# Kernel optimization log

Hardware: AMD Instinct MI355X
Metric: run time of the kernel (lower is better)

## Reference

```python
import jax, jax.numpy as jnp
import numpy as np

EPS = 1e-08  # matches torch default eps in both F.normalize and PairwiseDistance


def setup_inputs() -> dict:
    key = jax.random.key(0)
    x = jax.random.normal(key, (8192, 1024), dtype=jnp.float32)
    return {"x": x}


def reference(x) -> jnp.ndarray:
    B = x.shape[0]
    # F.normalize(x, p=2, dim=-1, eps=EPS): x / max(||x||_2, eps)
    norms = jnp.linalg.norm(x, axis=-1, keepdims=True)
    xn = x / jnp.maximum(norms, EPS)
    # cosine similarity matrix [B, B]
    cos_sim = xn @ xn.T
    # fill_diagonal_(-2): exclude self from nearest-neighbor search
    idx = jnp.arange(B)
    cos_sim = cos_sim.at[idx, idx].set(-2.0)
    nn_idx = jnp.argmax(cos_sim, axis=1)  # [B] int
    # torch PairwiseDistance(p=2, eps=EPS): ||x1 - x2 + eps||_2
    diff = xn - xn[nn_idx] + EPS
    nn_dist = jnp.sqrt(jnp.sum(diff * diff, axis=-1))  # [B]
    loss = -jnp.mean(jnp.log(nn_dist + EPS))
    return loss
```

## Files before the change

### kernel.cpp

```cpp
#include <hip/hip_runtime.h>
#include <hip/hip_bf16.h>
#include <math.h>

#define NB 8192
#define ND 1024
#define KEPS 1e-8f
#define SLOTS 128
#define NTIL 64
#define NWG 2080
#define NKT 32

typedef __attribute__((ext_vector_type(8))) __bf16 bf16x8;
typedef __attribute__((ext_vector_type(4))) float f32x4;

__device__ __forceinline__ unsigned int fmono(float f) {
    unsigned int b = __float_as_uint(f);
    return b ^ ((b & 0x80000000u) ? 0xFFFFFFFFu : 0x80000000u);
}
__device__ __forceinline__ unsigned short f2bf(float f) {
    union { float f; unsigned int u; } a;
    a.f = f;
    unsigned int lsb = (a.u >> 16) & 1u;
    a.u += 0x7fffu + lsb;
    return (unsigned short)(a.u >> 16);
}
__device__ __forceinline__ void gload_lds16(const void* g, void* l) {
    __builtin_amdgcn_global_load_lds(
        (const __attribute__((address_space(1))) unsigned int*)g,
        (__attribute__((address_space(3))) unsigned int*)l, 16, 0, 0);
}
__device__ __forceinline__ unsigned long long packmax(float mx, int mc) {
    return ((unsigned long long)fmono(mx) << 32) |
           (unsigned long long)(~(unsigned int)mc);
}

__global__ __launch_bounds__(256) void normalize_k(const float* __restrict__ x,
                                                   unsigned short* __restrict__ xnb) {
    int row = blockIdx.x * 4 + (threadIdx.x >> 6);
    int l = threadIdx.x & 63;
    const float4* xr = (const float4*)(x + (size_t)row * ND);
    float4 v[4];
    float ss = 0.f;
#pragma unroll
    for (int q = 0; q < 4; ++q) {
        v[q] = xr[q * 64 + l];
        ss += v[q].x * v[q].x + v[q].y * v[q].y + v[q].z * v[q].z + v[q].w * v[q].w;
    }
#pragma unroll
    for (int off = 1; off < 64; off <<= 1) ss += __shfl_xor(ss, off, 64);
    float scale = 1.0f / fmaxf(sqrtf(ss), KEPS);
    ushort4* o = (ushort4*)(xnb + (size_t)row * ND);
#pragma unroll
    for (int q = 0; q < 4; ++q) {
        ushort4 u;
        u.x = f2bf(v[q].x * scale);
        u.y = f2bf(v[q].y * scale);
        u.z = f2bf(v[q].z * scale);
        u.w = f2bf(v[q].w * scale);
        o[q * 64 + l] = u;
    }
}

#define FENCE_BARRIER() do { asm volatile("" ::: "memory"); \
    __builtin_amdgcn_s_barrier(); asm volatile("" ::: "memory"); } while (0)
#define WAIT_VM4() asm volatile("s_waitcnt vmcnt(4)" ::: "memory")
#define WAIT_VM0() asm volatile("s_waitcnt vmcnt(0)" ::: "memory")

#define STAGEALL(DB) do { \
    gload_lds16(spA0, ldsb + (DB) + (wv * 2 + 0) * 1024); \
    gload_lds16(spA1, ldsb + (DB) + (wv * 2 + 1) * 1024); \
    gload_lds16(spB0, ldsb + (DB) + 8192 + (wv * 2 + 0) * 1024); \
    gload_lds16(spB1, ldsb + (DB) + 8192 + (wv * 2 + 1) * 1024); \
    spA0 += 64; spA1 += 64; spB0 += 64; spB1 += 64; } while (0)

#define COMPUTE(CB) do { \
    bf16x8 af[4], bfr[4]; \
    _Pragma("unroll") for (int mi = 0; mi < 4; ++mi) \
        af[mi] = *(const bf16x8*)(ldsb + (CB) + wM * 4096 + mi * 1024 + rowks); \
    _Pragma("unroll") for (int ni = 0; ni < 4; ++ni) \
        bfr[ni] = *(const bf16x8*)(ldsb + (CB) + 8192 + wN * 4096 + ni * 1024 + rowks); \
    _Pragma("unroll") for (int mi = 0; mi < 4; ++mi) \
    _Pragma("unroll") for (int ni = 0; ni < 4; ++ni) \
        acc[mi][ni] = __builtin_amdgcn_mfma_f32_16x16x32_bf16(af[mi], bfr[ni], acc[mi][ni], 0, 0, 0); \
    } while (0)

#define KT(CB, SB) do { \
    WAIT_VM4(); FENCE_BARRIER(); STAGEALL(SB); COMPUTE(CB); } while (0)

__global__ __launch_bounds__(256, 3) void argmax_gemm(const unsigned short* __restrict__ xnb,
                                                      unsigned long long* __restrict__ partial) {
    __shared__ char ldsb[49152];

    int wg = (int)blockIdx.x;
    int tile = (wg & 7) * (NWG / 8) + (wg >> 3);
    int by = 0, tr = tile;
    while (tr >= NTIL - by) { tr -= NTIL - by; ++by; }
    const int bx = by + tr;

    const int rowBase = by * 128, colBase = bx * 128;
    const int tid = (int)threadIdx.x;
    const int wv = tid >> 6;
    const int l = tid & 63;
    const int wM = wv >> 1;
    const int wN = wv & 1;

    const int rowks = (l & 15) * 64 + (((l >> 4) * 16) ^ (((l >> 1) & 3) << 4));

    const int scol = (((l & 3) ^ ((l >> 3) & 3)) << 4);
    const char* xb = (const char*)xnb;
    const int r0 = (wv * 2 + 0) * 16 + (l >> 2);
    const int r1 = (wv * 2 + 1) * 16 + (l >> 2);
    const char* spA0 = xb + (size_t)(rowBase + r0) * 2048 + scol;
    const char* spA1 = xb + (size_t)(rowBase + r1) * 2048 + scol;
    const char* spB0 = xb + (size_t)(colBase + r0) * 2048 + scol;
    const char* spB1 = xb + (size_t)(colBase + r1) * 2048 + scol;

    f32x4 acc[4][4];
#pragma unroll
    for (int m = 0; m < 4; ++m)
#pragma unroll
        for (int n = 0; n < 4; ++n) acc[m][n] = f32x4{0.f, 0.f, 0.f, 0.f};

    STAGEALL(0);
    STAGEALL(16384);

    for (int g = 0; g < 10; ++g) {
        KT(0, 32768);
        KT(16384, 0);
        KT(32768, 16384);
    }
    WAIT_VM4(); FENCE_BARRIER(); COMPUTE(0);
    WAIT_VM0(); FENCE_BARRIER(); COMPUTE(16384);

#pragma unroll
    for (int mi = 0; mi < 4; ++mi) {
#pragma unroll
        for (int r = 0; r < 4; ++r) {
            int gi = rowBase + wM * 64 + mi * 16 + (l >> 4) * 4 + r;
            float mx = -3.0f;
            int mc = 0x7FFFFFFF;
#pragma unroll
            for (int ni = 0; ni < 4; ++ni) {
                int gj = colBase + wN * 64 + ni * 16 + (l & 15);
                float v = (gi == gj) ? -2.0f : acc[mi][ni][r];
                if (v > mx) { mx = v; mc = gj; }
            }
#pragma unroll
            for (int off = 1; off < 16; off <<= 1) {
                float omx = __shfl_xor(mx, off, 64);
                int omc = __shfl_xor(mc, off, 64);
                if (omx > mx || (omx == mx && omc < mc)) { mx = omx; mc = omc; }
            }
            if ((l & 15) == 0)
                partial[(size_t)gi * SLOTS + (bx - by) * 2 + wN] = packmax(mx, mc);
        }
    }
    if (bx > by) {
#pragma unroll
        for (int ni = 0; ni < 4; ++ni) {
            int gj = colBase + wN * 64 + ni * 16 + (l & 15);
            float mx = -3.0f;
            int mc = 0x7FFFFFFF;
#pragma unroll
            for (int mi = 0; mi < 4; ++mi) {
#pragma unroll
                for (int r = 0; r < 4; ++r) {
                    int gi = rowBase + wM * 64 + mi * 16 + (l >> 4) * 4 + r;
                    float v = (gi == gj) ? -2.0f : acc[mi][ni][r];
                    if (v > mx) { mx = v; mc = gi; }
                }
            }
#pragma unroll
            for (int off = 16; off < 64; off <<= 1) {
                float omx = __shfl_xor(mx, off, 64);
                int omc = __shfl_xor(mc, off, 64);
                if (omx > mx || (omx == mx && omc < mc)) { mx = omx; mc = omc; }
            }
            if ((l >> 4) == 0)
                partial[(size_t)gj * SLOTS + (NTIL - bx) * 2 + by * 2 + wM] = packmax(mx, mc);
        }
    }
}

__global__ __launch_bounds__(256) void dist_k(const float* __restrict__ x,
                                              const unsigned long long* __restrict__ partial,
                                              float* __restrict__ rowloss) {
    int i = blockIdx.x * 4 + (threadIdx.x >> 6);
    int l = threadIdx.x & 63;
    unsigned long long p = partial[(size_t)i * SLOTS + l];
    {
        unsigned long long o = partial[(size_t)i * SLOTS + l + 64];
        if (o > p) p = o;
    }
#pragma unroll
    for (int off = 1; off < 64; off <<= 1) {
        unsigned long long o = __shfl_xor(p, off, 64);
        if (o > p) p = o;
    }
    int j = (int)(~(unsigned int)(p & 0xFFFFFFFFull));

    const float4* xi = (const float4*)(x + (size_t)i * ND);
    const float4* xj = (const float4*)(x + (size_t)j * ND);
    float4 a[4], b[4];
    float sa = 0.f, sb = 0.f;
#pragma unroll
    for (int q = 0; q < 4; ++q) {
        a[q] = xi[q * 64 + l];
        b[q] = xj[q * 64 + l];
        sa += a[q].x * a[q].x + a[q].y * a[q].y + a[q].z * a[q].z + a[q].w * a[q].w;
        sb += b[q].x * b[q].x + b[q].y * b[q].y + b[q].z * b[q].z + b[q].w * b[q].w;
    }
#pragma unroll
    for (int off = 1; off < 64; off <<= 1) {
        sa += __shfl_xor(sa, off, 64);
        sb += __shfl_xor(sb, off, 64);
    }
    float ia = 1.0f / fmaxf(sqrtf(sa), KEPS);
    float ib = 1.0f / fmaxf(sqrtf(sb), KEPS);
    float ss = 0.f;
#pragma unroll
    for (int q = 0; q < 4; ++q) {
        float dx = a[q].x * ia - b[q].x * ib + KEPS;
        float dy = a[q].y * ia - b[q].y * ib + KEPS;
        float dz = a[q].z * ia - b[q].z * ib + KEPS;
        float dw = a[q].w * ia - b[q].w * ib + KEPS;
        ss += dx * dx + dy * dy + dz * dz + dw * dw;
    }
#pragma unroll
    for (int off = 1; off < 64; off <<= 1) ss += __shfl_xor(ss, off, 64);
    if (l == 0) rowloss[i] = -logf(sqrtf(ss) + KEPS);
}

__global__ __launch_bounds__(1024) void reduce_k(const float* __restrict__ rowloss,
                                                 float* __restrict__ out) {
    int t = threadIdx.x;
    float s = 0.0f;
#pragma unroll
    for (int k = 0; k < 8; ++k) s += rowloss[t + k * 1024];
#pragma unroll
    for (int off = 32; off > 0; off >>= 1) s += __shfl_down(s, off, 64);
    __shared__ float sred[16];
    if ((t & 63) == 0) sred[t >> 6] = s;
    __syncthreads();
    if (t == 0) {
        float tot = 0.0f;
        for (int k = 0; k < 16; ++k) tot += sred[k];
        out[0] = tot / (float)NB;
    }
}

extern "C" void kernel_launch(void* const* d_in, const int* in_sizes, int n_in,
                              void* d_out, int out_size, void* d_ws, size_t ws_size,
                              hipStream_t stream) {
    const float* x = (const float*)d_in[0];
    float* out = (float*)d_out;

    char* ws = (char*)d_ws;
    unsigned short* xnb = (unsigned short*)ws;
    unsigned long long* partial =
        (unsigned long long*)(ws + (size_t)NB * ND * 2);
    float* rowloss = (float*)(ws + (size_t)NB * ND * 2 + (size_t)NB * SLOTS * 8);

    normalize_k<<<NB / 4, 256, 0, stream>>>(x, xnb);
    argmax_gemm<<<NWG, 256, 0, stream>>>(xnb, partial);
    dist_k<<<NB / 4, 256, 0, stream>>>(x, partial, rowloss);
    reduce_k<<<1, 1024, 0, stream>>>(rowloss, out);
}
```

Measured before the change: 183.2 us.

## Compute neighbor distance algebraically from cached norms and argmax cosine value

Result: slower. 196.0 us (+7.0%).

```diff
diff --git a/kernel.cpp b/kernel.cpp
--- a/kernel.cpp
+++ b/kernel.cpp
@@ -17,6 +17,10 @@
     unsigned int b = __float_as_uint(f);
     return b ^ ((b & 0x80000000u) ? 0xFFFFFFFFu : 0x80000000u);
 }
+__device__ __forceinline__ float fmono_inv(unsigned int m) {
+    unsigned int b = (m & 0x80000000u) ? (m ^ 0x80000000u) : ~m;
+    return __uint_as_float(b);
+}
 __device__ __forceinline__ unsigned short f2bf(float f) {
     union { float f; unsigned int u; } a;
     a.f = f;
@@ -35,20 +39,28 @@
 }
 
 __global__ __launch_bounds__(256) void normalize_k(const float* __restrict__ x,
-                                                   unsigned short* __restrict__ xnb) {
+                                                   unsigned short* __restrict__ xnb,
+                                                   float2* __restrict__ sn,
+                                                   float* __restrict__ out) {
+    if (blockIdx.x == 0 && threadIdx.x == 0) out[0] = 0.0f;
     int row = blockIdx.x * 4 + (threadIdx.x >> 6);
     int l = threadIdx.x & 63;
     const float4* xr = (const float4*)(x + (size_t)row * ND);
     float4 v[4];
-    float ss = 0.f;
+    float ss = 0.f, sv = 0.f;
 #pragma unroll
     for (int q = 0; q < 4; ++q) {
         v[q] = xr[q * 64 + l];
         ss += v[q].x * v[q].x + v[q].y * v[q].y + v[q].z * v[q].z + v[q].w * v[q].w;
-    }
-#pragma unroll
-    for (int off = 1; off < 64; off <<= 1) ss += __shfl_xor(ss, off, 64);
+        sv += v[q].x + v[q].y + v[q].z + v[q].w;
+    }
+#pragma unroll
+    for (int off = 1; off < 64; off <<= 1) {
+        ss += __shfl_xor(ss, off, 64);
+        sv += __shfl_xor(sv, off, 64);
+    }
     float scale = 1.0f / fmaxf(sqrtf(ss), KEPS);
+    if (l == 0) sn[row] = make_float2(sv * scale, ss * scale * scale);
     ushort4* o = (ushort4*)(xnb + (size_t)row * ND);
 #pragma unroll
     for (int q = 0; q < 4; ++q) {
@@ -182,14 +194,14 @@
     }
 }
 
-__global__ __launch_bounds__(256) void dist_k(const float* __restrict__ x,
-                                              const unsigned long long* __restrict__ partial,
-                                              float* __restrict__ rowloss) {
+__global__ __launch_bounds__(256) void finalize_k(const unsigned long long* __restrict__ partial,
+                                                  const float2* __restrict__ sn,
+                                                  float* __restrict__ out) {
     int i = blockIdx.x * 4 + (threadIdx.x >> 6);
     int l = threadIdx.x & 63;
     unsigned long long p = partial[(size_t)i * SLOTS + l];
     {
-        unsigned long long o = partial[(size_t)i * SLOTS + l + 64];
+        unsigned long long o = partial[(size_t)i * SLOTS + 64 + l];
         if (o > p) p = o;
     }
 #pragma unroll
@@ -197,55 +209,19 @@
         unsigned long long o = __shfl_xor(p, off, 64);
         if (o > p) p = o;
     }
-    int j = (int)(~(unsigned int)(p & 0xFFFFFFFFull));
-
-    const float4* xi = (const float4*)(x + (size_t)i * ND);
-    const float4* xj = (const float4*)(x + (size_t)j * ND);
-    float4 a[4], b[4];
-    float sa = 0.f, sb = 0.f;
-#pragma unroll
-    for (int q = 0; q < 4; ++q) {
-        a[q] = xi[q * 64 + l];
-        b[q] = xj[q * 64 + l];
-        sa += a[q].x * a[q].x + a[q].y * a[q].y + a[q].z * a[q].z + a[q].w * a[q].w;
-        sb += b[q].x * b[q].x + b[q].y * b[q].y + b[q].z * b[q].z + b[q].w * b[q].w;
-    }
-#pragma unroll
-    for (int off = 1; off < 64; off <<= 1) {
-        sa += __shfl_xor(sa, off, 64);
-        sb += __shfl_xor(sb, off, 64);
-    }
-    float ia = 1.0f / fmaxf(sqrtf(sa), KEPS);
-    float ib = 1.0f / fmaxf(sqrtf(sb), KEPS);
-    float ss = 0.f;
-#pragma unroll
-    for (int q = 0; q < 4; ++q) {
-        float dx = a[q].x * ia - b[q].x * ib + KEPS;
-        float dy = a[q].y * ia - b[q].y * ib + KEPS;
-        float dz = a[q].z * ia - b[q].z * ib + KEPS;
-        float dw = a[q].w * ia - b[q].w * ib + KEPS;
-        ss += dx * dx + dy * dy + dz * dz + dw * dw;
-    }
-#pragma unroll
-    for (int off = 1; off < 64; off <<= 1) ss += __shfl_xor(ss, off, 64);
-    if (l == 0) rowloss[i] = -logf(sqrtf(ss) + KEPS);
-}
-
-__global__ __launch_bounds__(1024) void reduce_k(const float* __restrict__ rowloss,
-                                                 float* __restrict__ out) {
-    int t = threadIdx.x;
-    float s = 0.0f;
-#pragma unroll
-    for (int k = 0; k < 8; ++k) s += rowloss[t + k * 1024];
-#pragma unroll
-    for (int off = 32; off > 0; off >>= 1) s += __shfl_down(s, off, 64);
-    __shared__ float sred[16];
-    if ((t & 63) == 0) sred[t >> 6] = s;
+    __shared__ float red[4];
+    if (l == 0) {
+        float c = fmono_inv((unsigned int)(p >> 32));
+        int j = (int)(~(unsigned int)(p & 0xFFFFFFFFull));
+        float2 si = sn[i];
+        float2 sj = sn[j];
+        float d2 = si.y + sj.y - 2.0f * c + 2e-8f * (si.x - sj.x) + 1.024e-13f;
+        red[threadIdx.x >> 6] = logf(sqrtf(d2) + KEPS);
+    }
     __syncthreads();
-    if (t == 0) {
-        float tot = 0.0f;
-        for (int k = 0; k < 16; ++k) tot += sred[k];
-        out[0] = tot / (float)NB;
+    if (threadIdx.x == 0) {
+        float s = red[0] + red[1] + red[2] + red[3];
+        atomicAdd(out, -s * (1.0f / (float)NB));
     }
 }
 
@@ -259,10 +235,9 @@
     unsigned short* xnb = (unsigned short*)ws;
     unsigned long long* partial =
         (unsigned long long*)(ws + (size_t)NB * ND * 2);
-    float* rowloss = (float*)(ws + (size_t)NB * ND * 2 + (size_t)NB * SLOTS * 8);
-
-    normalize_k<<<NB / 4, 256, 0, stream>>>(x, xnb);
+    float2* sn = (float2*)(ws + (size_t)NB * ND * 2 + (size_t)NB * SLOTS * 8);
+
+    normalize_k<<<NB / 4, 256, 0, stream>>>(x, xnb, sn, out);
     argmax_gemm<<<NWG, 256, 0, stream>>>(xnb, partial);
-    dist_k<<<NB / 4, 256, 0, stream>>>(x, partial, rowloss);
-    reduce_k<<<1, 1024, 0, stream>>>(rowloss, out);
-}
+    finalize_k<<<NB / 4, 256, 0, stream>>>(partial, sn, out);
+}
```
